# Kernel optimization log

Hardware: AMD Instinct MI355X
Metric: run time of the kernel (lower is better)

Reference implementation:

```python
import jax, jax.numpy as jnp
import numpy as np

CONF_THRESH = 0.3
NMS_THRESH = 0.5
TOP_K = 64
VAR = (0.1, 0.2)  # standard SSD decode variances


def setup_inputs() -> dict:
    key = jax.random.key(0)
    k1, k2, k3 = jax.random.split(key, 3)
    B, A, C = 16, 16384, 81
    loc = jax.random.normal(k1, (B, A, 4), jnp.float32)
    conf = jax.random.normal(k2, (B, A, C), jnp.float32)
    anchors = jax.random.uniform(k3, (A, 4), jnp.float32)  # cxcywh in [0,1]
    return {"loc": loc, "conf": conf, "anchors": anchors}


def _decode(loc, anchors):
    # SSD-style decode: loc [A,4] offsets, anchors [A,4] cxcywh -> corners [A,4]
    cxcy = anchors[:, :2] + loc[:, :2] * VAR[0] * anchors[:, 2:]
    wh = anchors[:, 2:] * jnp.exp(loc[:, 2:] * VAR[1])
    tl = cxcy - wh * 0.5
    return jnp.concatenate([tl, tl + wh], axis=1)


def _iou(box, boxes):
    # box [4], boxes [A,4] in corner format
    tl = jnp.maximum(box[:2], boxes[:, :2])
    br = jnp.minimum(box[2:], boxes[:, 2:])
    wh = jnp.clip(br - tl, 0.0)
    inter = wh[:, 0] * wh[:, 1]
    a1 = (box[2] - box[0]) * (box[3] - box[1])
    a2 = (boxes[:, 2] - boxes[:, 0]) * (boxes[:, 3] - boxes[:, 1])
    return inter / (a1 + a2 - inter)


def _nms(boxes, scores):
    # greedy NMS for one (batch, class) lane; boxes [A,4], scores [A]
    s0 = jnp.where(scores > CONF_THRESH, scores, -1.0)

    def step(s, _):
        i = jnp.argmax(s)
        sc = s[i]
        box = boxes[i]
        keep = sc > 0.0  # -1 means masked/suppressed; valid scores > conf_thresh > 0
        supp = jnp.where(_iou(box, boxes) > NMS_THRESH, -1.0, s).at[i].set(-1.0)
        s_next = jnp.where(keep, supp, s)
        row = jnp.where(keep, jnp.concatenate([sc[None], box]),
                        jnp.zeros((5,), s.dtype))
        return s_next, row

    _, rows = jax.lax.scan(step, s0, None, length=TOP_K)
    return rows  # [TOP_K, 5] = (score, x1, y1, x2, y2), zero-padded


def reference(loc, conf, anchors):
    conf = jax.nn.sigmoid(conf)                      # [B,A,C]
    boxes = jax.vmap(_decode, in_axes=(0, None))(loc, anchors)  # [B,A,4]
    scores = jnp.swapaxes(conf, 1, 2)                # [B,C,A]
    per_class = jax.vmap(_nms, in_axes=(None, 0))    # over classes
    out = jax.vmap(per_class)(boxes, scores)         # [B,C,TOP_K,5]
    return out
```

## Files before the change

### kernel.cpp

```cpp
#include <hip/hip_runtime.h>
#include <math.h>

constexpr int B_N  = 16;
constexpr int A_N  = 16384;
constexpr int C_N  = 81;
constexpr int TOPK = 64;
constexpr int DNT  = 256;
constexpr int NBINS = 232;
constexpr int CAP   = 512;
constexpr unsigned BIN_BASE = 0x3E99u;

constexpr int TA   = 128;
constexpr int TPAD = 85;
constexpr int TNT  = 256;
constexpr int TILE_ELEMS = TA * C_N;
constexpr int TILE_F4    = (TA / 4) * C_N;

constexpr int SNT = 256;

__global__ __launch_bounds__(DNT) void decode_kernel(const float4* __restrict__ loc,
                                                     const float4* __restrict__ anch,
                                                     float4* __restrict__ boxes) {
    int i = blockIdx.x * DNT + threadIdx.x;
    int a = i & (A_N - 1);
    float4 l  = loc[i];
    float4 an = anch[a];
    float cx = an.x + (l.x * 0.1f) * an.z;
    float cy = an.y + (l.y * 0.1f) * an.w;
    float w  = an.z * expf(l.z * 0.2f);
    float h  = an.w * expf(l.w * 0.2f);
    float x1 = cx - w * 0.5f;
    float y1 = cy - h * 0.5f;
    boxes[i] = make_float4(x1, y1, x1 + w, y1 + h);
}

__global__ __launch_bounds__(TNT) void sigT_kernel(const float* __restrict__ conf,
                                                   float* __restrict__ scoresT) {
    __shared__ float tile[TA][TPAD];

    const int a0 = blockIdx.x * TA;
    const int b  = blockIdx.y;
    const int t  = threadIdx.x;

    const float* src = conf + ((size_t)b * A_N + a0) * C_N;
#pragma unroll
    for (int i = 0; i < (TILE_ELEMS + TNT - 1) / TNT; ++i) {
        int idx = i * TNT + t;
        if (idx < TILE_ELEMS) {
            float x  = src[idx];
            int   al = idx / C_N;
            int   cc = idx - al * C_N;
            tile[al][cc] = 1.0f / (1.0f + expf(-x));
        }
    }
    __syncthreads();
    float* dst = scoresT + (size_t)b * C_N * A_N + a0;
#pragma unroll
    for (int i = 0; i < (TILE_F4 + TNT - 1) / TNT; ++i) {
        int idx4 = i * TNT + t;
        if (idx4 < TILE_F4) {
            int cc  = idx4 >> 5;
            int al4 = idx4 & 31;
            float4 v;
            v.x = tile[al4 * 4 + 0][cc];
            v.y = tile[al4 * 4 + 1][cc];
            v.z = tile[al4 * 4 + 2][cc];
            v.w = tile[al4 * 4 + 3][cc];
            ((float4*)(dst + (size_t)cc * A_N))[al4] = v;
        }
    }
}

__global__ __launch_bounds__(SNT) void select_kernel(const float* __restrict__ scoresT,
                                                     int* __restrict__ ghist,
                                                     unsigned long long* __restrict__ gcand,
                                                     int2* __restrict__ gmeta) {
    __shared__ int hist[NBINS];
    __shared__ int s_cnt;
    const int bc = blockIdx.x;
    const int t  = threadIdx.x;
    for (int i = t; i < NBINS; i += SNT) hist[i] = 0;
    __syncthreads();

    const float4* sptr = (const float4*)(scoresT + (size_t)bc * A_N);
    for (int i = 0; i < A_N / 4 / SNT; ++i) {
        float4 s4 = sptr[t + SNT * i];
        float s[4] = {s4.x, s4.y, s4.z, s4.w};
#pragma unroll
        for (int q = 0; q < 4; ++q) {
            if (s[q] > 0.3f) {
                unsigned u = __float_as_uint(s[q]);
                int bin = (int)(u >> 16) - (int)BIN_BASE;
                bin = bin < 0 ? 0 : (bin > NBINS - 1 ? NBINS - 1 : bin);
                atomicAdd(&hist[bin], 1);
            }
        }
    }
    __syncthreads();
    int* g = ghist + (size_t)bc * NBINS;
    for (int i = t; i < NBINS; i += SNT) g[i] = hist[i];

    int lo = NBINS, tot = 0;
    while (lo > 0) {
        int cnt = hist[lo - 1];
        if (tot + cnt > CAP) {
            if (tot == 0) { lo--; }
            break;
        }
        tot += cnt; lo--;
    }
    if (t == 0) s_cnt = 0;
    __syncthreads();

    unsigned long long* cd = gcand + (size_t)bc * CAP;
    for (int i = 0; i < A_N / 4 / SNT; ++i) {
        float4 s4 = sptr[t + SNT * i];
        float s[4] = {s4.x, s4.y, s4.z, s4.w};
#pragma unroll
        for (int q = 0; q < 4; ++q) {
            if (s[q] > 0.3f) {
                unsigned u = __float_as_uint(s[q]);
                int bin = (int)(u >> 16) - (int)BIN_BASE;
                bin = bin < 0 ? 0 : (bin > NBINS - 1 ? NBINS - 1 : bin);
                if (bin >= lo) {
                    int slot = atomicAdd(&s_cnt, 1);
                    if (slot < CAP) {
                        unsigned a = (unsigned)(4 * (t + SNT * i) + q);
                        cd[slot] = ((unsigned long long)u << 32) | (unsigned)(~a);
                    }
                }
            }
        }
    }
    __syncthreads();
    if (t == 0) {
        int C = s_cnt; if (C > CAP) C = CAP;
        gmeta[bc] = make_int2(C, lo);
    }
}

__device__ __forceinline__ void sort_gather_scan(
        unsigned long long* cand, float4* cbox, int C, int lane,
        const float4* __restrict__ bptr, float* __restrict__ optr,
        float& rx1, float& ry1, float& rx2, float& ry2, float& rar,
        int& acc, int& kout) {
    unsigned long long key[8];
#pragma unroll
    for (int r = 0; r < 8; ++r) {
        int sidx = r * 64 + lane;
        key[r] = (sidx < C) ? cand[sidx] : 0ull;
    }
#pragma unroll
    for (int k = 2; k <= CAP; k <<= 1) {
#pragma unroll
        for (int j = k >> 1; j > 0; j >>= 1) {
            if (j >= 64) {
                int jr = j >> 6;
#pragma unroll
                for (int r = 0; r < 8; ++r) {
                    int rp = r ^ jr;
                    if (rp > r) {
                        int e = r * 64 + lane;
                        bool up = ((e & k) == 0);
                        unsigned long long va = key[r], vb = key[rp];
                        bool sw = up ? (va < vb) : (va > vb);
                        if (sw) { key[r] = vb; key[rp] = va; }
                    }
                }
            } else {
#pragma unroll
                for (int r = 0; r < 8; ++r) {
                    int e = r * 64 + lane;
                    bool up    = ((e & k) == 0);
                    bool isLow = ((lane & j) == 0);
                    unsigned long long va = key[r];
                    unsigned long long vb = __shfl_xor(va, j, 64);
                    bool keepMax = (up == isLow);
                    key[r] = keepMax ? (va > vb ? va : vb)
                                     : (va < vb ? va : vb);
                }
            }
        }
    }
    __syncthreads();
#pragma unroll
    for (int r = 0; r < 8; ++r) cand[r * 64 + lane] = key[r];
    __syncthreads();
#pragma unroll
    for (int r = 0; r < 8; ++r) {
        int e = r * 64 + lane;
        if (e < C) cbox[e] = bptr[(int)(~(unsigned)cand[e])];
    }
    __syncthreads();

    int t = 0;
    unsigned long long k0 = cand[0];
    float4 cb = cbox[0];
    while (t < C) {
        unsigned long long nk = 0ull;
        float4 nb = cb;
        if (t + 1 < C) { nk = cand[t + 1]; nb = cbox[t + 1]; }
        float sc = __uint_as_float((unsigned)(k0 >> 32));
        float ca = (cb.z - cb.x) * (cb.w - cb.y);
        bool over = false;
        if (lane < acc) {
            float tlx = fmaxf(rx1, cb.x);
            float tly = fmaxf(ry1, cb.y);
            float brx = fminf(rx2, cb.z);
            float bry = fminf(ry2, cb.w);
            float iw  = fmaxf(brx - tlx, 0.0f);
            float ih  = fmaxf(bry - tly, 0.0f);
            float inter = iw * ih;
            float iou = inter / (rar + ca - inter);
            over = iou > 0.5f;
        }
        if (!__any(over)) {
            if (lane == acc) { rx1 = cb.x; ry1 = cb.y; rx2 = cb.z; ry2 = cb.w; rar = ca; }
            if (lane == 0) {
                float* o = optr + (size_t)kout * 5;
                o[0] = sc; o[1] = cb.x; o[2] = cb.y; o[3] = cb.z; o[4] = cb.w;
            }
            acc++; kout++;
            if (acc == TOPK) break;
        }
        ++t; k0 = nk; cb = nb;
    }
}

template <bool PRESEL>
__global__ __launch_bounds__(64, 4) void nms_kernel(const float* __restrict__ conf,
                                                    const float* __restrict__ scoresT,
                                                    const int* __restrict__ ghist,
                                                    const unsigned long long* __restrict__ gcand,
                                                    const int2* __restrict__ gmeta,
                                                    const float4* __restrict__ boxes,
                                                    float* __restrict__ out) {
    __shared__ int hist[NBINS];
    __shared__ unsigned long long cand[CAP];
    __shared__ float4 cbox[CAP];
    __shared__ int s_cnt;

    const int c    = blockIdx.x;
    const int b    = blockIdx.y;
    const int bc   = b * C_N + c;
    const int lane = threadIdx.x;

    const float4* bptr = boxes + (size_t)b * A_N;
    const float4* sptr = (const float4*)(scoresT + (size_t)bc * A_N);
    const float*  cptr = conf + (size_t)b * A_N * C_N + c;
    float* optr = out + (size_t)bc * TOPK * 5;

    float rx1 = 0.f, ry1 = 0.f, rx2 = 0.f, ry2 = 0.f, rar = 0.f;
    int acc = 0, kout = 0;
    int bin_hi;

    if (PRESEL) {
        int2 meta = gmeta[bc];
        int C = meta.x;
        bin_hi = meta.y;
        const unsigned long long* cd = gcand + (size_t)bc * CAP;
#pragma unroll
        for (int r = 0; r < 8; ++r) {
            int e = r * 64 + lane;
            cand[e] = (e < C) ? cd[e] : 0ull;
        }
        __syncthreads();
        if (C > 0)
            sort_gather_scan(cand, cbox, C, lane, bptr, optr,
                             rx1, ry1, rx2, ry2, rar, acc, kout);
        if (acc < TOPK && bin_hi > 0) {
            for (int i = lane; i < NBINS; i += 64) hist[i] = ghist[(size_t)bc * NBINS + i];
            __syncthreads();
        }
    } else {
        for (int i = lane; i < NBINS; i += 64) hist[i] = 0;
        __syncthreads();
        for (int i = 0; i < A_N / 256; ++i) {
            int a0 = 4 * (lane + 64 * i);
#pragma unroll
            for (int q = 0; q < 4; ++q) {
                float x = cptr[(size_t)(a0 + q) * C_N];
                float s = 1.0f / (1.0f + expf(-x));
                if (s > 0.3f) {
                    unsigned u = __float_as_uint(s);
                    int bin = (int)(u >> 16) - (int)BIN_BASE;
                    bin = bin < 0 ? 0 : (bin > NBINS - 1 ? NBINS - 1 : bin);
                    atomicAdd(&hist[bin], 1);
                }
            }
        }
        __syncthreads();
        bin_hi = NBINS;
    }

    while (acc < TOPK) {
        int lo = bin_hi, tot = 0;
        while (lo > 0) {
            int cnt = hist[lo - 1];
            if (tot + cnt > CAP) {
                if (tot == 0) { lo--; }
                break;
            }
            tot += cnt; lo--;
        }
        const int bin_lo = lo;
        if (bin_lo == bin_hi) break;
        if (lane == 0) s_cnt = 0;
        __syncthreads();

        for (int i = 0; i < A_N / 256; ++i) {
            float s[4];
            if (PRESEL) {
                float4 s4 = sptr[lane + 64 * i];
                s[0] = s4.x; s[1] = s4.y; s[2] = s4.z; s[3] = s4.w;
            } else {
                int a0 = 4 * (lane + 64 * i);
#pragma unroll
                for (int q = 0; q < 4; ++q) {
                    float x = cptr[(size_t)(a0 + q) * C_N];
                    s[q] = 1.0f / (1.0f + expf(-x));
                }
            }
#pragma unroll
            for (int q = 0; q < 4; ++q) {
                if (s[q] > 0.3f) {
                    unsigned u = __float_as_uint(s[q]);
                    int bin = (int)(u >> 16) - (int)BIN_BASE;
                    bin = bin < 0 ? 0 : (bin > NBINS - 1 ? NBINS - 1 : bin);
                    if (bin >= bin_lo && bin < bin_hi) {
                        int slot = atomicAdd(&s_cnt, 1);
                        if (slot < CAP) {
                            unsigned a = (unsigned)(4 * (lane + 64 * i) + q);
                            cand[slot] = ((unsigned long long)u << 32) | (unsigned)(~a);
                        }
                    }
                }
            }
        }
        __syncthreads();
        int C = s_cnt; if (C > CAP) C = CAP;
        if (C > 0)
            sort_gather_scan(cand, cbox, C, lane, bptr, optr,
                             rx1, ry1, rx2, ry2, rar, acc, kout);
        bin_hi = bin_lo;
    }

    {
        float* o  = optr + (size_t)kout * 5;
        int   rem = (TOPK - kout) * 5;
        for (int t = lane; t < rem; t += 64) o[t] = 0.0f;
    }
}

extern "C" void kernel_launch(void* const* d_in, const int* in_sizes, int n_in,
                              void* d_out, int out_size, void* d_ws, size_t ws_size,
                              hipStream_t stream) {
    const float* loc     = (const float*)d_in[0];
    const float* conf    = (const float*)d_in[1];
    const float* anchors = (const float*)d_in[2];
    float* out = (float*)d_out;

    const size_t boxes_bytes  = (size_t)B_N * A_N * sizeof(float4);
    const size_t scores_bytes = (size_t)B_N * C_N * A_N * sizeof(float);
    const size_t hist_bytes   = (size_t)B_N * C_N * NBINS * sizeof(int);
    const size_t cand_bytes   = (size_t)B_N * C_N * CAP * sizeof(unsigned long long);
    const size_t meta_bytes   = (size_t)B_N * C_N * sizeof(int2);

    float4* boxes = (float4*)d_ws;

    decode_kernel<<<(B_N * A_N) / DNT, DNT, 0, stream>>>(
        (const float4*)loc, (const float4*)anchors, boxes);

    if (ws_size >= boxes_bytes + scores_bytes + hist_bytes + cand_bytes + meta_bytes) {
        char* p = (char*)d_ws + boxes_bytes;
        float* scoresT            = (float*)p;              p += scores_bytes;
        int*   ghist              = (int*)p;                p += hist_bytes;
        unsigned long long* gcand = (unsigned long long*)p; p += cand_bytes;
        int2*  gmeta              = (int2*)p;
        sigT_kernel<<<dim3(A_N / TA, B_N), TNT, 0, stream>>>(conf, scoresT);
        select_kernel<<<dim3(B_N * C_N), SNT, 0, stream>>>(scoresT, ghist, gcand, gmeta);
        nms_kernel<true><<<dim3(C_N, B_N), 64, 0, stream>>>(conf, scoresT, ghist, gcand, gmeta, boxes, out);
    } else {
        nms_kernel<false><<<dim3(C_N, B_N), 64, 0, stream>>>(conf, nullptr, nullptr, nullptr, nullptr, boxes, out);
    }
}
```

Baseline: 224.7 us.

## Fuse select and NMS into one 256-thread kernel per class lane

```diff
diff --git a/kernel.cpp b/kernel.cpp
--- a/kernel.cpp
+++ b/kernel.cpp
@@ -10,7 +10,7 @@
 constexpr int CAP   = 512;
 constexpr unsigned BIN_BASE = 0x3E99u;
 
-constexpr int TA   = 128;
+constexpr int TA   = 64;
 constexpr int TPAD = 85;
 constexpr int TNT  = 256;
 constexpr int TILE_ELEMS = TA * C_N;
@@ -59,8 +59,8 @@
     for (int i = 0; i < (TILE_F4 + TNT - 1) / TNT; ++i) {
         int idx4 = i * TNT + t;
         if (idx4 < TILE_F4) {
-            int cc  = idx4 >> 5;
-            int al4 = idx4 & 31;
+            int cc  = idx4 >> 4;
+            int al4 = idx4 & 15;
             float4 v;
             v.x = tile[al4 * 4 + 0][cc];
             v.y = tile[al4 * 4 + 1][cc];
@@ -71,18 +71,29 @@
     }
 }
 
-__global__ __launch_bounds__(SNT) void select_kernel(const float* __restrict__ scoresT,
-                                                     int* __restrict__ ghist,
-                                                     unsigned long long* __restrict__ gcand,
-                                                     int2* __restrict__ gmeta) {
+__global__ __launch_bounds__(SNT, 4) void select_nms_kernel(
+        const float* __restrict__ scoresT,
+        const float4* __restrict__ boxes,
+        float* __restrict__ out) {
     __shared__ int hist[NBINS];
-    __shared__ int s_cnt;
-    const int bc = blockIdx.x;
-    const int t  = threadIdx.x;
+    __shared__ unsigned long long cand[CAP];
+    __shared__ float4 cbox[CAP];
+    __shared__ int s_cnt, s_acc, s_kout;
+
+    const int bc   = blockIdx.x;
+    const int b    = bc / C_N;
+    const int t    = threadIdx.x;
+    const int lane = t & 63;
+    const int wv   = t >> 6;
+
     for (int i = t; i < NBINS; i += SNT) hist[i] = 0;
+    if (t == 0) { s_acc = 0; s_kout = 0; }
     __syncthreads();
 
     const float4* sptr = (const float4*)(scoresT + (size_t)bc * A_N);
+    const float4* bptr = boxes + (size_t)b * A_N;
+    float* optr = out + (size_t)bc * TOPK * 5;
+
     for (int i = 0; i < A_N / 4 / SNT; ++i) {
         float4 s4 = sptr[t + SNT * i];
         float s[4] = {s4.x, s4.y, s4.z, s4.w};
@@ -97,49 +108,147 @@
         }
     }
     __syncthreads();
-    int* g = ghist + (size_t)bc * NBINS;
-    for (int i = t; i < NBINS; i += SNT) g[i] = hist[i];
-
-    int lo = NBINS, tot = 0;
-    while (lo > 0) {
-        int cnt = hist[lo - 1];
-        if (tot + cnt > CAP) {
-            if (tot == 0) { lo--; }
-            break;
-        }
-        tot += cnt; lo--;
-    }
-    if (t == 0) s_cnt = 0;
-    __syncthreads();
-
-    unsigned long long* cd = gcand + (size_t)bc * CAP;
-    for (int i = 0; i < A_N / 4 / SNT; ++i) {
-        float4 s4 = sptr[t + SNT * i];
-        float s[4] = {s4.x, s4.y, s4.z, s4.w};
-#pragma unroll
-        for (int q = 0; q < 4; ++q) {
-            if (s[q] > 0.3f) {
-                unsigned u = __float_as_uint(s[q]);
-                int bin = (int)(u >> 16) - (int)BIN_BASE;
-                bin = bin < 0 ? 0 : (bin > NBINS - 1 ? NBINS - 1 : bin);
-                if (bin >= lo) {
-                    int slot = atomicAdd(&s_cnt, 1);
-                    if (slot < CAP) {
-                        unsigned a = (unsigned)(4 * (t + SNT * i) + q);
-                        cd[slot] = ((unsigned long long)u << 32) | (unsigned)(~a);
-                    }
-                }
-            }
-        }
-    }
-    __syncthreads();
-    if (t == 0) {
+
+    float rx1 = 0.f, ry1 = 0.f, rx2 = 0.f, ry2 = 0.f, rar = 0.f;
+    int acc = 0, kout = 0;
+
+    int bin_hi = NBINS;
+    for (;;) {
+        int lo = bin_hi, tot = 0;
+        while (lo > 0) {
+            int cnt = hist[lo - 1];
+            if (tot + cnt > CAP) {
+                if (tot == 0) { lo--; }
+                break;
+            }
+            tot += cnt; lo--;
+        }
+        const int bin_lo = lo;
+        if (bin_lo == bin_hi) break;
+        if (t == 0) s_cnt = 0;
+        __syncthreads();
+
+        for (int i = 0; i < A_N / 4 / SNT; ++i) {
+            float4 s4 = sptr[t + SNT * i];
+            float s[4] = {s4.x, s4.y, s4.z, s4.w};
+#pragma unroll
+            for (int q = 0; q < 4; ++q) {
+                if (s[q] > 0.3f) {
+                    unsigned u = __float_as_uint(s[q]);
+                    int bin = (int)(u >> 16) - (int)BIN_BASE;
+                    bin = bin < 0 ? 0 : (bin > NBINS - 1 ? NBINS - 1 : bin);
+                    if (bin >= bin_lo && bin < bin_hi) {
+                        int slot = atomicAdd(&s_cnt, 1);
+                        if (slot < CAP) {
+                            unsigned a = (unsigned)(4 * (t + SNT * i) + q);
+                            cand[slot] = ((unsigned long long)u << 32) | (unsigned)(~a);
+                        }
+                    }
+                }
+            }
+        }
+        __syncthreads();
         int C = s_cnt; if (C > CAP) C = CAP;
-        gmeta[bc] = make_int2(C, lo);
-    }
-}
-
-__device__ __forceinline__ void sort_gather_scan(
+
+        if (C > 0) {
+            if (wv == 0) {
+                unsigned long long key[8];
+#pragma unroll
+                for (int r = 0; r < 8; ++r) {
+                    int sidx = r * 64 + lane;
+                    key[r] = (sidx < C) ? cand[sidx] : 0ull;
+                }
+#pragma unroll
+                for (int k = 2; k <= CAP; k <<= 1) {
+#pragma unroll
+                    for (int j = k >> 1; j > 0; j >>= 1) {
+                        if (j >= 64) {
+                            int jr = j >> 6;
+#pragma unroll
+                            for (int r = 0; r < 8; ++r) {
+                                int rp = r ^ jr;
+                                if (rp > r) {
+                                    int e = r * 64 + lane;
+                                    bool up = ((e & k) == 0);
+                                    unsigned long long va = key[r], vb = key[rp];
+                                    bool sw = up ? (va < vb) : (va > vb);
+                                    if (sw) { key[r] = vb; key[rp] = va; }
+                                }
+                            }
+                        } else {
+#pragma unroll
+                            for (int r = 0; r < 8; ++r) {
+                                int e = r * 64 + lane;
+                                bool up    = ((e & k) == 0);
+                                bool isLow = ((lane & j) == 0);
+                                unsigned long long va = key[r];
+                                unsigned long long vb = __shfl_xor(va, j, 64);
+                                bool keepMax = (up == isLow);
+                                key[r] = keepMax ? (va > vb ? va : vb)
+                                                 : (va < vb ? va : vb);
+                            }
+                        }
+                    }
+                }
+#pragma unroll
+                for (int r = 0; r < 8; ++r) cand[r * 64 + lane] = key[r];
+            }
+            __syncthreads();
+
+            for (int e = t; e < CAP; e += SNT)
+                if (e < C) cbox[e] = bptr[(int)(~(unsigned)cand[e])];
+            __syncthreads();
+
+            if (wv == 0) {
+                int ts = 0;
+                unsigned long long k0 = cand[0];
+                float4 cb = cbox[0];
+                while (ts < C) {
+                    unsigned long long nk = 0ull;
+                    float4 nb = cb;
+                    if (ts + 1 < C) { nk = cand[ts + 1]; nb = cbox[ts + 1]; }
+                    float sc = __uint_as_float((unsigned)(k0 >> 32));
+                    float ca = (cb.z - cb.x) * (cb.w - cb.y);
+                    bool over = false;
+                    if (lane < acc) {
+                        float tlx = fmaxf(rx1, cb.x);
+                        float tly = fmaxf(ry1, cb.y);
+                        float brx = fminf(rx2, cb.z);
+                        float bry = fminf(ry2, cb.w);
+                        float iw  = fmaxf(brx - tlx, 0.0f);
+                        float ih  = fmaxf(bry - tly, 0.0f);
+                        float inter = iw * ih;
+                        float iou = inter / (rar + ca - inter);
+                        over = iou > 0.5f;
+                    }
+                    if (!__any(over)) {
+                        if (lane == acc) { rx1 = cb.x; ry1 = cb.y; rx2 = cb.z; ry2 = cb.w; rar = ca; }
+                        if (lane == 0) {
+                            float* o = optr + (size_t)kout * 5;
+                            o[0] = sc; o[1] = cb.x; o[2] = cb.y; o[3] = cb.z; o[4] = cb.w;
+                        }
+                        acc++; kout++;
+                        if (acc == TOPK) break;
+                    }
+                    ++ts; k0 = nk; cb = nb;
+                }
+                if (lane == 0) { s_acc = acc; s_kout = kout; }
+            }
+            __syncthreads();
+            if (s_acc >= TOPK) break;
+        }
+        bin_hi = bin_lo;
+    }
+
+    {
+        const int ko = s_kout;
+        float* o  = optr + (size_t)ko * 5;
+        int   rem = (TOPK - ko) * 5;
+        for (int i = t; i < rem; i += SNT) o[i] = 0.0f;
+    }
+}
+
+__device__ __forceinline__ void sort_gather_scan64(
         unsigned long long* cand, float4* cbox, int C, int lane,
         const float4* __restrict__ bptr, float* __restrict__ optr,
         float& rx1, float& ry1, float& rx2, float& ry2, float& rar,
@@ -176,8 +285,7 @@
                     unsigned long long va = key[r];
                     unsigned long long vb = __shfl_xor(va, j, 64);
                     bool keepMax = (up == isLow);
-                    key[r] = keepMax ? (va > vb ? va : vb)
-                                     : (va < vb ? va : vb);
+                    key[r] = keepMax ? (va > vb ? va : vb) : (va < vb ? va : vb);
                 }
             }
         }
@@ -227,14 +335,9 @@
     }
 }
 
-template <bool PRESEL>
-__global__ __launch_bounds__(64, 4) void nms_kernel(const float* __restrict__ conf,
-                                                    const float* __restrict__ scoresT,
-                                                    const int* __restrict__ ghist,
-                                                    const unsigned long long* __restrict__ gcand,
-                                                    const int2* __restrict__ gmeta,
-                                                    const float4* __restrict__ boxes,
-                                                    float* __restrict__ out) {
+__global__ __launch_bounds__(64, 4) void nms_fallback(const float* __restrict__ conf,
+                                                      const float4* __restrict__ boxes,
+                                                      float* __restrict__ out) {
     __shared__ int hist[NBINS];
     __shared__ unsigned long long cand[CAP];
     __shared__ float4 cbox[CAP];
@@ -242,38 +345,43 @@
 
     const int c    = blockIdx.x;
     const int b    = blockIdx.y;
-    const int bc   = b * C_N + c;
     const int lane = threadIdx.x;
 
     const float4* bptr = boxes + (size_t)b * A_N;
-    const float4* sptr = (const float4*)(scoresT + (size_t)bc * A_N);
     const float*  cptr = conf + (size_t)b * A_N * C_N + c;
-    float* optr = out + (size_t)bc * TOPK * 5;
+    float* optr = out + (size_t)(b * C_N + c) * TOPK * 5;
+
+    for (int i = lane; i < NBINS; i += 64) hist[i] = 0;
+    __syncthreads();
+    for (int i = 0; i < A_N / 256; ++i) {
+        int a0 = 4 * (lane + 64 * i);
+#pragma unroll
+        for (int q = 0; q < 4; ++q) {
+            float x = cptr[(size_t)(a0 + q) * C_N];
+            float s = 1.0f / (1.0f + expf(-x));
+            if (s > 0.3f) {
+                unsigned u = __float_as_uint(s);
+                int bin = (int)(u >> 16) - (int)BIN_BASE;
+                bin = bin < 0 ? 0 : (bin > NBINS - 1 ? NBINS - 1 : bin);
+                atomicAdd(&hist[bin], 1);
+            }
+        }
+    }
+    __syncthreads();
 
     float rx1 = 0.f, ry1 = 0.f, rx2 = 0.f, ry2 = 0.f, rar = 0.f;
     int acc = 0, kout = 0;
-    int bin_hi;
-
-    if (PRESEL) {
-        int2 meta = gmeta[bc];
-        int C = meta.x;
-        bin_hi = meta.y;
-        const unsigned long long* cd = gcand + (size_t)bc * CAP;
-#pragma unroll
-        for (int r = 0; r < 8; ++r) {
-            int e = r * 64 + lane;
-            cand[e] = (e < C) ? cd[e] : 0ull;
-        }
-        __syncthreads();
-        if (C > 0)
-            sort_gather_scan(cand, cbox, C, lane, bptr, optr,
-                             rx1, ry1, rx2, ry2, rar, acc, kout);
-        if (acc < TOPK && bin_hi > 0) {
-            for (int i = lane; i < NBINS; i += 64) hist[i] = ghist[(size_t)bc * NBINS + i];
-            __syncthreads();
-        }
-    } else {
-        for (int i = lane; i < NBINS; i += 64) hist[i] = 0;
+    int bin_hi = NBINS;
+    for (;;) {
+        int lo = bin_hi, tot = 0;
+        while (lo > 0) {
+            int cnt = hist[lo - 1];
+            if (tot + cnt > CAP) { if (tot == 0) { lo--; } break; }
+            tot += cnt; lo--;
+        }
+        const int bin_lo = lo;
+        if (bin_lo == bin_hi) break;
+        if (lane == 0) s_cnt = 0;
         __syncthreads();
         for (int i = 0; i < A_N / 256; ++i) {
             int a0 = 4 * (lane + 64 * i);
@@ -285,54 +393,10 @@
                     unsigned u = __float_as_uint(s);
                     int bin = (int)(u >> 16) - (int)BIN_BASE;
                     bin = bin < 0 ? 0 : (bin > NBINS - 1 ? NBINS - 1 : bin);
-                    atomicAdd(&hist[bin], 1);
-                }
-            }
-        }
-        __syncthreads();
-        bin_hi = NBINS;
-    }
-
-    while (acc < TOPK) {
-        int lo = bin_hi, tot = 0;
-        while (lo > 0) {
-            int cnt = hist[lo - 1];
-            if (tot + cnt > CAP) {
-                if (tot == 0) { lo--; }
-                break;
-            }
-            tot += cnt; lo--;
-        }
-        const int bin_lo = lo;
-        if (bin_lo == bin_hi) break;
-        if (lane == 0) s_cnt = 0;
-        __syncthreads();
-
-        for (int i = 0; i < A_N / 256; ++i) {
-            float s[4];
-            if (PRESEL) {
-                float4 s4 = sptr[lane + 64 * i];
-                s[0] = s4.x; s[1] = s4.y; s[2] = s4.z; s[3] = s4.w;
-            } else {
-                int a0 = 4 * (lane + 64 * i);
-#pragma unroll
-                for (int q = 0; q < 4; ++q) {
-                    float x = cptr[(size_t)(a0 + q) * C_N];
-                    s[q] = 1.0f / (1.0f + expf(-x));
-                }
-            }
-#pragma unroll
-            for (int q = 0; q < 4; ++q) {
-                if (s[q] > 0.3f) {
-                    unsigned u = __float_as_uint(s[q]);
-                    int bin = (int)(u >> 16) - (int)BIN_BASE;
-                    bin = bin < 0 ? 0 : (bin > NBINS - 1 ? NBINS - 1 : bin);
                     if (bin >= bin_lo && bin < bin_hi) {
                         int slot = atomicAdd(&s_cnt, 1);
-                        if (slot < CAP) {
-                            unsigned a = (unsigned)(4 * (lane + 64 * i) + q);
-                            cand[slot] = ((unsigned long long)u << 32) | (unsigned)(~a);
-                        }
+                        if (slot < CAP)
+                            cand[slot] = ((unsigned long long)u << 32) | (unsigned)(~(unsigned)(a0 + q));
                     }
                 }
             }
@@ -340,15 +404,15 @@
         __syncthreads();
         int C = s_cnt; if (C > CAP) C = CAP;
         if (C > 0)
-            sort_gather_scan(cand, cbox, C, lane, bptr, optr,
-                             rx1, ry1, rx2, ry2, rar, acc, kout);
+            sort_gather_scan64(cand, cbox, C, lane, bptr, optr,
+                               rx1, ry1, rx2, ry2, rar, acc, kout);
+        if (acc == TOPK) break;
         bin_hi = bin_lo;
     }
-
     {
         float* o  = optr + (size_t)kout * 5;
         int   rem = (TOPK - kout) * 5;
-        for (int t = lane; t < rem; t += 64) o[t] = 0.0f;
+        for (int i = lane; i < rem; i += 64) o[i] = 0.0f;
     }
 }
 
@@ -362,25 +426,17 @@
 
     const size_t boxes_bytes  = (size_t)B_N * A_N * sizeof(float4);
     const size_t scores_bytes = (size_t)B_N * C_N * A_N * sizeof(float);
-    const size_t hist_bytes   = (size_t)B_N * C_N * NBINS * sizeof(int);
-    const size_t cand_bytes   = (size_t)B_N * C_N * CAP * sizeof(unsigned long long);
-    const size_t meta_bytes   = (size_t)B_N * C_N * sizeof(int2);
 
     float4* boxes = (float4*)d_ws;
 
     decode_kernel<<<(B_N * A_N) / DNT, DNT, 0, stream>>>(
         (const float4*)loc, (const float4*)anchors, boxes);
 
-    if (ws_size >= boxes_bytes + scores_bytes + hist_bytes + cand_bytes + meta_bytes) {
-        char* p = (char*)d_ws + boxes_bytes;
-        float* scoresT            = (float*)p;              p += scores_bytes;
-        int*   ghist              = (int*)p;                p += hist_bytes;
-        unsigned long long* gcand = (unsigned long long*)p; p += cand_bytes;
-        int2*  gmeta              = (int2*)p;
+    if (ws_size >= boxes_bytes + scores_bytes) {
+        float* scoresT = (float*)((char*)d_ws + boxes_bytes);
         sigT_kernel<<<dim3(A_N / TA, B_N), TNT, 0, stream>>>(conf, scoresT);
-        select_kernel<<<dim3(B_N * C_N), SNT, 0, stream>>>(scoresT, ghist, gcand, gmeta);
-        nms_kernel<true><<<dim3(C_N, B_N), 64, 0, stream>>>(conf, scoresT, ghist, gcand, gmeta, boxes, out);
+        select_nms_kernel<<<dim3(B_N * C_N), SNT, 0, stream>>>(scoresT, boxes, out);
     } else {
-        nms_kernel<false><<<dim3(C_N, B_N), 64, 0, stream>>>(conf, nullptr, nullptr, nullptr, nullptr, boxes, out);
-    }
-}
+        nms_fallback<<<dim3(C_N, B_N), 64, 0, stream>>>(conf, boxes, out);
+    }
+}
```

New measurement: 220.7 us. About the same (-1.8%).
